# Kernel optimization log

Hardware: AMD Instinct MI355X
Metric: run time of the kernel (lower is better)

The kernel has to match this reference:

```python
import jax, jax.numpy as jnp
import numpy as np

B = 64        # images
P = 100       # boxes per image
C = 256       # q_in_dim
ST = 9        # spatiotemporal_size
M = 2048      # memory entries per image
L = 2         # attention blocks
H = 8         # heads
QK = 256      # qk_out_dim
V = 256       # v_out_dim
FF = 1024     # ff hidden
TEMP = 1.0
SCALER = 1.0 / (TEMP * float(np.sqrt(QK // H)))
EPS = 1e-5


def _ln(x, g, b):
    mu = x.mean(-1, keepdims=True)
    var = ((x - mu) ** 2).mean(-1, keepdims=True)
    return (x - mu) * jax.lax.rsqrt(var + EPS) * g + b


def setup_inputs() -> dict:
    key = jax.random.key(0)
    ks = jax.random.split(key, 32)
    s = 0.02
    KV = C + ST
    d = {
        "features": jax.random.normal(ks[0], (B * P, C, 7, 7), jnp.float32),
        "memory": jax.random.normal(ks[1], (B, M, KV), jnp.float32),
        "Wq": jax.random.normal(ks[2], (L, C, QK), jnp.float32) * s,
        "bq": jnp.zeros((L, QK), jnp.float32),
        "Wk": jax.random.normal(ks[3], (L, KV, QK), jnp.float32) * s,
        "bk": jnp.zeros((L, QK), jnp.float32),
        "Wv": jax.random.normal(ks[4], (L, KV, V), jnp.float32) * s,
        "bv": jnp.zeros((L, V), jnp.float32),
        "Wf": jax.random.normal(ks[5], (L, V, C), jnp.float32) * s,
        "bf": jnp.zeros((L, C), jnp.float32),
        "g1": jnp.ones((L, C), jnp.float32),
        "be1": jnp.zeros((L, C), jnp.float32),
        "g2": jnp.ones((L, C), jnp.float32),
        "be2": jnp.zeros((L, C), jnp.float32),
        "W1": jax.random.normal(ks[6], (L, C, FF), jnp.float32) * s,
        "b1": jnp.zeros((L, FF), jnp.float32),
        "W2": jax.random.normal(ks[7], (L, FF, C), jnp.float32) * s,
        "b2": jnp.zeros((L, C), jnp.float32),
        "Wp1": jax.random.normal(ks[8], (C, FF), jnp.float32) * s,
        "bp1": jnp.zeros((FF,), jnp.float32),
        "Wp2": jax.random.normal(ks[9], (FF, C), jnp.float32) * s,
        "bp2": jnp.zeros((C,), jnp.float32),
        "boxes_per_image": P,
    }
    return d


def reference(features, memory, Wq, bq, Wk, bk, Wv, bv, Wf, bf,
              g1, be1, g2, be2, W1, b1, W2, b2, Wp1, bp1, Wp2, bp2,
              boxes_per_image):
    nb, nm = memory.shape[0], memory.shape[1]
    p = boxes_per_image
    # avg_pool2d(kernel=7) on 7x7 -> spatial mean
    z = features.mean(axis=(2, 3))  # [N, C]
    for i in range(Wq.shape[0]):
        zb = z.reshape(nb, p, -1)                              # [B,P,C]
        q = (zb @ Wq[i] + bq[i]).reshape(nb, p, H, -1)         # [B,P,H,dh]
        k = (memory @ Wk[i] + bk[i]).reshape(nb, nm, H, -1)    # [B,M,H,dh]
        v = (memory @ Wv[i] + bv[i]).reshape(nb, nm, H, -1)
        w = jax.nn.softmax(jnp.einsum('bphd,bmhd->bphm', q, k) * SCALER, axis=-1)
        wv = jnp.einsum('bphm,bmhd->bphd', w, v).reshape(nb, p, -1)
        f = (wv @ Wf[i] + bf[i]).reshape(nb * p, -1)           # [N,C]
        z = _ln(z + f, g1[i], be1[i])
        ff = jnp.maximum(z @ W1[i] + b1[i], 0.0) @ W2[i] + b2[i]
        z = _ln(z + ff, g2[i], be2[i])
    z = jnp.maximum(z @ Wp1 + bp1, 0.0) @ Wp2 + bp2            # ff_post
    return features + z[:, :, None, None]
```

## Files before the change

kernel.cpp:

```cpp
#include <hip/hip_runtime.h>
#include <hip/hip_bf16.h>

typedef __hip_bfloat16 bf16;
typedef float f32x4 __attribute__((ext_vector_type(4)));
typedef short s16x8 __attribute__((ext_vector_type(8)));

#define SCALER_F 0.17677669529663687f

__global__ __launch_bounds__(256) void pool_kernel(
    const float* __restrict__ feat, float* __restrict__ z, bf16* __restrict__ zb) {
  __shared__ float ls[12544];
  const int n = blockIdx.x, t = threadIdx.x;
  const float* fp = feat + (long)n * 12544;
#pragma unroll
  for (int e = t, i = 0; i < 49; i++, e += 256) ls[e] = fp[e];
  __syncthreads();
  float s = 0.f;
  const float* r = ls + t * 49;
#pragma unroll
  for (int i = 0; i < 49; i++) s += r[i];
  s *= (1.f / 49.f);
  z[n * 256 + t] = s;
  zb[n * 256 + t] = __float2bfloat16(s);
}

__global__ __launch_bounds__(64) void transpose_bf(
    const float* __restrict__ src, bf16* __restrict__ dst, int K, int N, int Kpad) {
  const int n = blockIdx.x, t = threadIdx.x;
  for (int k = t; k < Kpad; k += 64)
    dst[(long)n * Kpad + k] = __float2bfloat16(k < K ? src[(long)k * N + n] : 0.f);
}

__global__ __launch_bounds__(64) void conv_mem(
    const float* __restrict__ mem, bf16* __restrict__ mb) {
  const long r = blockIdx.x;
  const int t = threadIdx.x;
  for (int c = t; c < 288; c += 64)
    mb[r * 288 + c] = __float2bfloat16(c < 265 ? mem[r * 265 + c] : 0.f);
}

__global__ void concat_bias(const float* __restrict__ bk, const float* __restrict__ bv,
                            float* __restrict__ kvbias) {
  int i = blockIdx.x * 256 + threadIdx.x;
  if (i < 1024) {
    int l = i >> 9, c = i & 511;
    kvbias[i] = (c < 256) ? bk[l * 256 + c] : bv[l * 256 + c - 256];
  }
}

__global__ __launch_bounds__(256, 2) void gemm_bt(
    const bf16* __restrict__ A, const bf16* __restrict__ Bt,
    const float* __restrict__ bias, float* __restrict__ Cf, bf16* __restrict__ Cb,
    int K, int lda, int ldb, int ldc, float scale, int relu) {
  __shared__ bf16 Als[128 * 32];
  __shared__ bf16 Bls[128 * 32];
  const int m0 = blockIdx.x * 128;
  const int n0 = blockIdx.y * 128;
  const int t = threadIdx.x;
  const int w = t >> 6, lane = t & 63;
  const int rw = (w >> 1) * 64, cw = (w & 1) * 64;
  const int l15 = lane & 15, quad = lane >> 4;

  f32x4 zero4 = {0.f, 0.f, 0.f, 0.f};
  f32x4 acc[4][4];
#pragma unroll
  for (int i = 0; i < 4; i++)
#pragma unroll
    for (int j = 0; j < 4; j++) acc[i][j] = zero4;

  const bf16* Ab = A + (long)m0 * lda;
  const bf16* Bb = Bt + (long)n0 * ldb;
  const int r1 = t >> 2, s1 = t & 3;

  for (int k0 = 0; k0 < K; k0 += 32) {
    __syncthreads();
    __builtin_amdgcn_global_load_lds(
        (const __attribute__((address_space(1))) void*)(Ab + (long)r1 * lda + k0 + s1 * 8),
        (__attribute__((address_space(3))) void*)(Als + t * 8), 16, 0, 0);
    __builtin_amdgcn_global_load_lds(
        (const __attribute__((address_space(1))) void*)(Ab + (long)(r1 + 64) * lda + k0 + s1 * 8),
        (__attribute__((address_space(3))) void*)(Als + 2048 + t * 8), 16, 0, 0);
    __builtin_amdgcn_global_load_lds(
        (const __attribute__((address_space(1))) void*)(Bb + (long)r1 * ldb + k0 + s1 * 8),
        (__attribute__((address_space(3))) void*)(Bls + t * 8), 16, 0, 0);
    __builtin_amdgcn_global_load_lds(
        (const __attribute__((address_space(1))) void*)(Bb + (long)(r1 + 64) * ldb + k0 + s1 * 8),
        (__attribute__((address_space(3))) void*)(Bls + 2048 + t * 8), 16, 0, 0);
    __syncthreads();

    s16x8 af[4], bfr[4];
#pragma unroll
    for (int i = 0; i < 4; i++) {
      af[i]  = *(const s16x8*)(Als + (rw + i * 16 + l15) * 32 + quad * 8);
      bfr[i] = *(const s16x8*)(Bls + (cw + i * 16 + l15) * 32 + quad * 8);
    }
#pragma unroll
    for (int i = 0; i < 4; i++)
#pragma unroll
      for (int j = 0; j < 4; j++)
        acc[i][j] = __builtin_amdgcn_mfma_f32_16x16x32_bf16(af[i], bfr[j], acc[i][j], 0, 0, 0);
  }

#pragma unroll
  for (int i = 0; i < 4; i++) {
    const int row = m0 + rw + i * 16 + quad * 4;
#pragma unroll
    for (int j = 0; j < 4; j++) {
      const int col = n0 + cw + j * 16 + l15;
      const float bvv = bias ? bias[col] : 0.f;
#pragma unroll
      for (int r = 0; r < 4; r++) {
        float v = (acc[i][j][r] + bvv) * scale;
        if (relu) v = fmaxf(v, 0.f);
        const long off = (long)(row + r) * ldc + col;
        if (Cb) Cb[off] = __float2bfloat16(v);
        else    Cf[off] = v;
      }
    }
  }
}

__global__ __launch_bounds__(256) void attn_kernel(
    const bf16* __restrict__ q, const bf16* __restrict__ kv, bf16* __restrict__ wv) {
  const int h = blockIdx.x;
  const int b = blockIdx.y;
  const int t = threadIdx.x;
  const int w = t >> 6, lane = t & 63;
  const int l15 = lane & 15, quad = lane >> 4;

  __shared__ bf16 Kls[64 * 32];
  __shared__ bf16 Vtls[32 * 72];
  __shared__ bf16 Pls[4][16 * 72];

  s16x8 aQ[2];
  f32x4 zero4 = {0.f, 0.f, 0.f, 0.f};
  f32x4 o[2][2];
  float lsum[2][4];
#pragma unroll
  for (int i = 0; i < 2; i++) {
    o[i][0] = zero4; o[i][1] = zero4;
#pragma unroll
    for (int r = 0; r < 4; r++) lsum[i][r] = 0.f;
  }
#pragma unroll
  for (int qt = 0; qt < 2; qt++) {
    const int row = (2 * w + qt) * 16 + l15;
    s16x8 tmp = {0, 0, 0, 0, 0, 0, 0, 0};
    if (row < 100)
      tmp = *(const s16x8*)(q + ((long)(b * 100 + row)) * 256 + h * 32 + quad * 8);
    aQ[qt] = tmp;
  }

  const bf16* kvb = kv + (long)b * 2048 * 512;
  const int sr = t >> 2, ss = t & 3;

  for (int mc = 0; mc < 2048; mc += 64) {
    __syncthreads();
    {
      const uint4 gk = *(const uint4*)(kvb + (long)(mc + sr) * 512 + h * 32 + ss * 8);
      *(uint4*)(Kls + sr * 32 + ss * 8) = gk;
      const uint4 gv = *(const uint4*)(kvb + (long)(mc + sr) * 512 + 256 + h * 32 + ss * 8);
      const bf16* vs = (const bf16*)&gv;
#pragma unroll
      for (int j = 0; j < 8; j++) Vtls[(ss * 8 + j) * 72 + sr] = vs[j];
    }
    __syncthreads();

    s16x8 bk[4], bv00, bv01, bv10, bv11;
#pragma unroll
    for (int f = 0; f < 4; f++)
      bk[f] = *(const s16x8*)(Kls + (f * 16 + l15) * 32 + quad * 8);
    bv00 = *(const s16x8*)(Vtls + l15 * 72 + quad * 8);
    bv01 = *(const s16x8*)(Vtls + l15 * 72 + 32 + quad * 8);
    bv10 = *(const s16x8*)(Vtls + (16 + l15) * 72 + quad * 8);
    bv11 = *(const s16x8*)(Vtls + (16 + l15) * 72 + 32 + quad * 8);

#pragma unroll
    for (int qt = 0; qt < 2; qt++) {
      f32x4 s_[4];
#pragma unroll
      for (int f = 0; f < 4; f++)
        s_[f] = __builtin_amdgcn_mfma_f32_16x16x32_bf16(aQ[qt], bk[f], zero4, 0, 0, 0);
#pragma unroll
      for (int f = 0; f < 4; f++) {
#pragma unroll
        for (int r = 0; r < 4; r++) {
          const float pv = __expf(s_[f][r]);
          lsum[qt][r] += pv;
          Pls[w][(quad * 4 + r) * 72 + f * 16 + l15] = __float2bfloat16(pv);
        }
      }
      __threadfence_block();
      const s16x8 aP0 = *(const s16x8*)(&Pls[w][0] + l15 * 72 + quad * 8);
      const s16x8 aP1 = *(const s16x8*)(&Pls[w][0] + l15 * 72 + 32 + quad * 8);
      o[qt][0] = __builtin_amdgcn_mfma_f32_16x16x32_bf16(aP0, bv00, o[qt][0], 0, 0, 0);
      o[qt][0] = __builtin_amdgcn_mfma_f32_16x16x32_bf16(aP1, bv01, o[qt][0], 0, 0, 0);
      o[qt][1] = __builtin_amdgcn_mfma_f32_16x16x32_bf16(aP0, bv10, o[qt][1], 0, 0, 0);
      o[qt][1] = __builtin_amdgcn_mfma_f32_16x16x32_bf16(aP1, bv11, o[qt][1], 0, 0, 0);
    }
  }

#pragma unroll
  for (int qt = 0; qt < 2; qt++) {
    const int gq = (2 * w + qt) * 16;
#pragma unroll
    for (int r = 0; r < 4; r++) {
      float l = lsum[qt][r];
      l += __shfl_xor(l, 1); l += __shfl_xor(l, 2);
      l += __shfl_xor(l, 4); l += __shfl_xor(l, 8);
      const float inv = 1.f / l;
      const int qrow = gq + quad * 4 + r;
      if (qrow < 100) {
        const long base = ((long)(b * 100 + qrow)) * 256 + h * 32;
        wv[base + l15]      = __float2bfloat16(o[qt][0][r] * inv);
        wv[base + 16 + l15] = __float2bfloat16(o[qt][1][r] * inv);
      }
    }
  }
}

__global__ __launch_bounds__(64) void ln_kernel(
    float* __restrict__ z, const float* __restrict__ d,
    const float* __restrict__ g, const float* __restrict__ be, bf16* __restrict__ zb) {
  const int row = blockIdx.x, t = threadIdx.x;
  float4 x = *(const float4*)(z + (long)row * 256 + t * 4);
  const float4 dd = *(const float4*)(d + (long)row * 256 + t * 4);
  x.x += dd.x; x.y += dd.y; x.z += dd.z; x.w += dd.w;
  float s1 = x.x + x.y + x.z + x.w;
  float s2 = x.x * x.x + x.y * x.y + x.z * x.z + x.w * x.w;
#pragma unroll
  for (int m = 1; m < 64; m <<= 1) {
    s1 += __shfl_xor(s1, m);
    s2 += __shfl_xor(s2, m);
  }
  const float mu = s1 * (1.f / 256.f);
  const float var = s2 * (1.f / 256.f) - mu * mu;
  const float rs = rsqrtf(var + 1e-5f);
  const float4 gg = *(const float4*)(g + t * 4);
  const float4 bb = *(const float4*)(be + t * 4);
  float4 y;
  y.x = (x.x - mu) * rs * gg.x + bb.x;
  y.y = (x.y - mu) * rs * gg.y + bb.y;
  y.z = (x.z - mu) * rs * gg.z + bb.z;
  y.w = (x.w - mu) * rs * gg.w + bb.w;
  *(float4*)(z + (long)row * 256 + t * 4) = y;
  bf16* zo = zb + (long)row * 256 + t * 4;
  zo[0] = __float2bfloat16(y.x); zo[1] = __float2bfloat16(y.y);
  zo[2] = __float2bfloat16(y.z); zo[3] = __float2bfloat16(y.w);
}

__global__ __launch_bounds__(256) void final_add(
    const float* __restrict__ feat, const float* __restrict__ zp, float* __restrict__ out) {
  const int n = blockIdx.x, t = threadIdx.x;
  const long base = (long)n * 12544;
#pragma unroll
  for (int idx = t, i = 0; i < 49; i++, idx += 256) {
    const int c = idx / 49;
    out[base + idx] = feat[base + idx] + zp[n * 256 + c];
  }
}

extern "C" void kernel_launch(void* const* d_in, const int* in_sizes, int n_in,
                              void* d_out, int out_size, void* d_ws, size_t ws_size,
                              hipStream_t stream) {
  (void)in_sizes; (void)n_in; (void)out_size; (void)ws_size;
  const float* features = (const float*)d_in[0];
  const float* memory_  = (const float*)d_in[1];
  const float* Wq_  = (const float*)d_in[2];
  const float* bq_  = (const float*)d_in[3];
  const float* Wk_  = (const float*)d_in[4];
  const float* bk_  = (const float*)d_in[5];
  const float* Wv_  = (const float*)d_in[6];
  const float* bv_  = (const float*)d_in[7];
  const float* Wf_  = (const float*)d_in[8];
  const float* bf_  = (const float*)d_in[9];
  const float* g1_  = (const float*)d_in[10];
  const float* be1_ = (const float*)d_in[11];
  const float* g2_  = (const float*)d_in[12];
  const float* be2_ = (const float*)d_in[13];
  const float* W1_  = (const float*)d_in[14];
  const float* b1_  = (const float*)d_in[15];
  const float* W2_  = (const float*)d_in[16];
  const float* b2_  = (const float*)d_in[17];
  const float* Wp1_ = (const float*)d_in[18];
  const float* bp1_ = (const float*)d_in[19];
  const float* Wp2_ = (const float*)d_in[20];
  const float* bp2_ = (const float*)d_in[21];
  float* out = (float*)d_out;

  char* p = (char*)d_ws;
  auto alloc = [&](size_t bytes) {
    char* r = p;
    p += (bytes + 255) & ~(size_t)255;
    return r;
  };
  float* z     = (float*)alloc((size_t)6400 * 256 * 4);
  float* fb    = (float*)alloc((size_t)6400 * 256 * 4);
  bf16*  zb    = (bf16*)alloc((size_t)6400 * 256 * 2);
  bf16*  qb    = (bf16*)alloc((size_t)6400 * 256 * 2);
  bf16*  wvb   = (bf16*)alloc((size_t)6400 * 256 * 2);
  bf16*  hb    = (bf16*)alloc((size_t)6400 * 1024 * 2);
  bf16*  memb  = (bf16*)alloc((size_t)131072 * 288 * 2);
  bf16*  kvbuf = (bf16*)alloc((size_t)131072 * 512 * 2);
  bf16*  wkvT  = (bf16*)alloc((size_t)2 * 512 * 288 * 2);
  bf16*  wqT   = (bf16*)alloc((size_t)2 * 256 * 256 * 2);
  bf16*  wfT   = (bf16*)alloc((size_t)2 * 256 * 256 * 2);
  bf16*  w1T   = (bf16*)alloc((size_t)2 * 1024 * 256 * 2);
  bf16*  w2T   = (bf16*)alloc((size_t)2 * 256 * 1024 * 2);
  bf16*  wp1T  = (bf16*)alloc((size_t)1024 * 256 * 2);
  bf16*  wp2T  = (bf16*)alloc((size_t)256 * 1024 * 2);
  float* kvbias = (float*)alloc((size_t)1024 * 4);

  conv_mem<<<131072, 64, 0, stream>>>(memory_, memb);
  for (int l = 0; l < 2; l++) {
    transpose_bf<<<256, 64, 0, stream>>>(Wk_ + (long)l * 265 * 256, wkvT + (long)l * 512 * 288, 265, 256, 288);
    transpose_bf<<<256, 64, 0, stream>>>(Wv_ + (long)l * 265 * 256, wkvT + (long)l * 512 * 288 + 256 * 288, 265, 256, 288);
    transpose_bf<<<256, 64, 0, stream>>>(Wq_ + (long)l * 256 * 256, wqT + (long)l * 256 * 256, 256, 256, 256);
    transpose_bf<<<256, 64, 0, stream>>>(Wf_ + (long)l * 256 * 256, wfT + (long)l * 256 * 256, 256, 256, 256);
    transpose_bf<<<1024, 64, 0, stream>>>(W1_ + (long)l * 256 * 1024, w1T + (long)l * 1024 * 256, 256, 1024, 256);
    transpose_bf<<<256, 64, 0, stream>>>(W2_ + (long)l * 1024 * 256, w2T + (long)l * 256 * 1024, 1024, 256, 1024);
  }
  transpose_bf<<<1024, 64, 0, stream>>>(Wp1_, wp1T, 256, 1024, 256);
  transpose_bf<<<256, 64, 0, stream>>>(Wp2_, wp2T, 1024, 256, 1024);
  concat_bias<<<4, 256, 0, stream>>>(bk_, bv_, kvbias);

  pool_kernel<<<6400, 256, 0, stream>>>(features, z, zb);

  for (int l = 0; l < 2; l++) {
    gemm_bt<<<dim3(1024, 4), 256, 0, stream>>>(memb, wkvT + (long)l * 512 * 288,
        kvbias + l * 512, nullptr, kvbuf, 288, 288, 288, 512, 1.f, 0);
    gemm_bt<<<dim3(50, 2), 256, 0, stream>>>(zb, wqT + (long)l * 256 * 256,
        bq_ + l * 256, nullptr, qb, 256, 256, 256, 256, SCALER_F, 0);
    attn_kernel<<<dim3(8, 64), 256, 0, stream>>>(qb, kvbuf, wvb);
    gemm_bt<<<dim3(50, 2), 256, 0, stream>>>(wvb, wfT + (long)l * 256 * 256,
        bf_ + l * 256, fb, nullptr, 256, 256, 256, 256, 1.f, 0);
    ln_kernel<<<6400, 64, 0, stream>>>(z, fb, g1_ + l * 256, be1_ + l * 256, zb);
    gemm_bt<<<dim3(50, 8), 256, 0, stream>>>(zb, w1T + (long)l * 1024 * 256,
        b1_ + l * 1024, nullptr, hb, 256, 256, 256, 1024, 1.f, 1);
    gemm_bt<<<dim3(50, 2), 256, 0, stream>>>(hb, w2T + (long)l * 256 * 1024,
        b2_ + l * 256, fb, nullptr, 1024, 1024, 1024, 256, 1.f, 0);
    ln_kernel<<<6400, 64, 0, stream>>>(z, fb, g2_ + l * 256, be2_ + l * 256, zb);
  }

  gemm_bt<<<dim3(50, 8), 256, 0, stream>>>(zb, wp1T, bp1_, nullptr, hb,
      256, 256, 256, 1024, 1.f, 1);
  gemm_bt<<<dim3(50, 2), 256, 0, stream>>>(hb, wp2T, bp2_, fb,
      nullptr, 1024, 1024, 1024, 256, 1.f, 0);

  final_add<<<6400, 256, 0, stream>>>(features, fb, out);
}
```

Measured before the change: 1.325 ms.

## Fuse prep kernels, batch KV projections, double-buffer attention, vectorize epilogues

Merges the memory conversion, weight transposes and bias concat into one prep kernel with vectorized memory reads. Runs both layers' K/V projections as a single wider GEMM into a 1024-column buffer. Double-buffers K/V tiles in the attention kernel so the next tile's global loads overlap compute. Swaps MFMA operand order so the GEMM epilogue writes 4-wide vectors, and vectorizes the pool and final-add kernels. Costs a larger KV buffer and a strided layer offset in attention.

Result: faster. 1.261 ms (-4.8%).

```diff
diff --git a/kernel.cpp b/kernel.cpp
--- a/kernel.cpp
+++ b/kernel.cpp
@@ -4,16 +4,98 @@
 typedef __hip_bfloat16 bf16;
 typedef float f32x4 __attribute__((ext_vector_type(4)));
 typedef short s16x8 __attribute__((ext_vector_type(8)));
+typedef unsigned short u16x4 __attribute__((ext_vector_type(4)));
 
 #define SCALER_F 0.17677669529663687f
+
+#define MEM_BLKS 33920
+#define PAD_BLKS 11776
+
+__global__ __launch_bounds__(256) void prep_kernel(
+    const float* __restrict__ mem, bf16* __restrict__ mb,
+    const float* __restrict__ Wq, const float* __restrict__ Wk,
+    const float* __restrict__ Wv, const float* __restrict__ Wf,
+    const float* __restrict__ W1, const float* __restrict__ W2,
+    const float* __restrict__ Wp1, const float* __restrict__ Wp2,
+    const float* __restrict__ bk, const float* __restrict__ bv,
+    bf16* __restrict__ wqT, bf16* __restrict__ wkvT, bf16* __restrict__ wfT,
+    bf16* __restrict__ w1T, bf16* __restrict__ w2T,
+    bf16* __restrict__ wp1T, bf16* __restrict__ wp2T,
+    float* __restrict__ kvbias) {
+  int bid = blockIdx.x;
+  const int t = threadIdx.x;
+  if (bid < MEM_BLKS) {
+    const long g4 = (long)bid * 256 + t;
+    const f32x4 v = *(const f32x4*)(mem + g4 * 4);
+    long g = g4 * 4;
+    unsigned r = (unsigned)(g / 265);
+    unsigned c = (unsigned)(g - (long)r * 265);
+#pragma unroll
+    for (int j = 0; j < 4; j++) {
+      mb[(long)r * 288 + c] = __float2bfloat16(v[j]);
+      if (++c == 265) { c = 0; r++; }
+    }
+    return;
+  }
+  bid -= MEM_BLKS;
+  if (bid < PAD_BLKS) {
+    const int p = bid * 256 + t;
+    const int r = p / 23, c = 265 + p % 23;
+    mb[(long)r * 288 + c] = __float2bfloat16(0.f);
+    return;
+  }
+  bid -= PAD_BLKS;
+  const float* src; bf16* dst; int K, N, n, Kpad;
+  if (bid < 1024) {
+    const int l = bid >> 9, pt = (bid >> 8) & 1; n = bid & 255;
+    src = (pt ? Wv : Wk) + (long)l * 265 * 256;
+    dst = wkvT + (long)l * 512 * 288 + (long)pt * 256 * 288;
+    K = 265; N = 256; Kpad = 288;
+  } else if (bid < 1536) {
+    const int i2 = bid - 1024, l = i2 >> 8; n = i2 & 255;
+    src = Wq + (long)l * 65536; dst = wqT + (long)l * 65536;
+    K = 256; N = 256; Kpad = 256;
+  } else if (bid < 2048) {
+    const int i2 = bid - 1536, l = i2 >> 8; n = i2 & 255;
+    src = Wf + (long)l * 65536; dst = wfT + (long)l * 65536;
+    K = 256; N = 256; Kpad = 256;
+  } else if (bid < 4096) {
+    const int i2 = bid - 2048, l = i2 >> 10; n = i2 & 1023;
+    src = W1 + (long)l * 262144; dst = w1T + (long)l * 262144;
+    K = 256; N = 1024; Kpad = 256;
+  } else if (bid < 4608) {
+    const int i2 = bid - 4096, l = i2 >> 8; n = i2 & 255;
+    src = W2 + (long)l * 262144; dst = w2T + (long)l * 262144;
+    K = 1024; N = 256; Kpad = 1024;
+  } else if (bid < 5632) {
+    n = bid - 4608; src = Wp1; dst = wp1T; K = 256; N = 1024; Kpad = 256;
+  } else if (bid < 5888) {
+    n = bid - 5632; src = Wp2; dst = wp2T; K = 1024; N = 256; Kpad = 1024;
+  } else {
+    for (int i = t; i < 1024; i += 256) {
+      const int l = i >> 9, c = i & 511;
+      kvbias[i] = (c < 256) ? bk[l * 256 + c] : bv[l * 256 + c - 256];
+    }
+    return;
+  }
+  for (int k = t; k < Kpad; k += 256)
+    dst[(long)n * Kpad + k] = __float2bfloat16(k < K ? src[(long)k * N + n] : 0.f);
+}
 
 __global__ __launch_bounds__(256) void pool_kernel(
     const float* __restrict__ feat, float* __restrict__ z, bf16* __restrict__ zb) {
   __shared__ float ls[12544];
   const int n = blockIdx.x, t = threadIdx.x;
-  const float* fp = feat + (long)n * 12544;
-#pragma unroll
-  for (int e = t, i = 0; i < 49; i++, e += 256) ls[e] = fp[e];
+  const f32x4* f4 = (const f32x4*)(feat + (long)n * 12544);
+#pragma unroll
+  for (int i = 0; i < 12; i++) {
+    const int e = i * 256 + t;
+    *(f32x4*)&ls[e * 4] = f4[e];
+  }
+  if (t < 64) {
+    const int e = 3072 + t;
+    *(f32x4*)&ls[e * 4] = f4[e];
+  }
   __syncthreads();
   float s = 0.f;
   const float* r = ls + t * 49;
@@ -22,30 +104,6 @@
   s *= (1.f / 49.f);
   z[n * 256 + t] = s;
   zb[n * 256 + t] = __float2bfloat16(s);
-}
-
-__global__ __launch_bounds__(64) void transpose_bf(
-    const float* __restrict__ src, bf16* __restrict__ dst, int K, int N, int Kpad) {
-  const int n = blockIdx.x, t = threadIdx.x;
-  for (int k = t; k < Kpad; k += 64)
-    dst[(long)n * Kpad + k] = __float2bfloat16(k < K ? src[(long)k * N + n] : 0.f);
-}
-
-__global__ __launch_bounds__(64) void conv_mem(
-    const float* __restrict__ mem, bf16* __restrict__ mb) {
-  const long r = blockIdx.x;
-  const int t = threadIdx.x;
-  for (int c = t; c < 288; c += 64)
-    mb[r * 288 + c] = __float2bfloat16(c < 265 ? mem[r * 265 + c] : 0.f);
-}
-
-__global__ void concat_bias(const float* __restrict__ bk, const float* __restrict__ bv,
-                            float* __restrict__ kvbias) {
-  int i = blockIdx.x * 256 + threadIdx.x;
-  if (i < 1024) {
-    int l = i >> 9, c = i & 511;
-    kvbias[i] = (c < 256) ? bk[l * 256 + c] : bv[l * 256 + c - 256];
-  }
 }
 
 __global__ __launch_bounds__(256, 2) void gemm_bt(
@@ -98,38 +156,50 @@
     for (int i = 0; i < 4; i++)
 #pragma unroll
       for (int j = 0; j < 4; j++)
-        acc[i][j] = __builtin_amdgcn_mfma_f32_16x16x32_bf16(af[i], bfr[j], acc[i][j], 0, 0, 0);
+        acc[i][j] = __builtin_amdgcn_mfma_f32_16x16x32_bf16(bfr[j], af[i], acc[i][j], 0, 0, 0);
   }
 
 #pragma unroll
   for (int i = 0; i < 4; i++) {
-    const int row = m0 + rw + i * 16 + quad * 4;
+    const long rb = (long)(m0 + rw + i * 16 + l15) * ldc;
 #pragma unroll
     for (int j = 0; j < 4; j++) {
-      const int col = n0 + cw + j * 16 + l15;
-      const float bvv = bias ? bias[col] : 0.f;
+      const int colb = n0 + cw + j * 16 + quad * 4;
+      f32x4 bv4 = {0.f, 0.f, 0.f, 0.f};
+      if (bias) bv4 = *(const f32x4*)(bias + colb);
+      f32x4 v;
 #pragma unroll
       for (int r = 0; r < 4; r++) {
-        float v = (acc[i][j][r] + bvv) * scale;
-        if (relu) v = fmaxf(v, 0.f);
-        const long off = (long)(row + r) * ldc + col;
-        if (Cb) Cb[off] = __float2bfloat16(v);
-        else    Cf[off] = v;
+        float x = (acc[i][j][r] + bv4[r]) * scale;
+        if (relu) x = fmaxf(x, 0.f);
+        v[r] = x;
       }
+      if (Cb) {
+        u16x4 u;
+#pragma unroll
+        for (int r = 0; r < 4; r++) {
+          bf16 tb = __float2bfloat16(v[r]);
+          u[r] = *(unsigned short*)&tb;
+        }
+        *(u16x4*)(Cb + rb + colb) = u;
+      } else {
+        *(f32x4*)(Cf + rb + colb) = v;
+      }
     }
   }
 }
 
 __global__ __launch_bounds__(256) void attn_kernel(
-    const bf16* __restrict__ q, const bf16* __restrict__ kv, bf16* __restrict__ wv) {
+    const bf16* __restrict__ q, const bf16* __restrict__ kv, bf16* __restrict__ wv,
+    int loff) {
   const int h = blockIdx.x;
   const int b = blockIdx.y;
   const int t = threadIdx.x;
   const int w = t >> 6, lane = t & 63;
   const int l15 = lane & 15, quad = lane >> 4;
 
-  __shared__ bf16 Kls[64 * 32];
-  __shared__ bf16 Vtls[32 * 72];
+  __shared__ bf16 Kls[2][64 * 32];
+  __shared__ bf16 Vtls[2][32 * 72];
   __shared__ bf16 Pls[4][16 * 72];
 
   s16x8 aQ[2];
@@ -151,29 +221,36 @@
     aQ[qt] = tmp;
   }
 
-  const bf16* kvb = kv + (long)b * 2048 * 512;
+  const bf16* kvb = kv + (long)b * 2048 * 1024 + loff;
   const int sr = t >> 2, ss = t & 3;
 
+  {
+    const uint4 gk = *(const uint4*)(kvb + (long)sr * 1024 + h * 32 + ss * 8);
+    *(uint4*)(&Kls[0][sr * 32 + ss * 8]) = gk;
+    const uint4 gv = *(const uint4*)(kvb + (long)sr * 1024 + 256 + h * 32 + ss * 8);
+    const bf16* vs = (const bf16*)&gv;
+#pragma unroll
+    for (int j = 0; j < 8; j++) Vtls[0][(ss * 8 + j) * 72 + sr] = vs[j];
+  }
+  __syncthreads();
+
+  int cur = 0;
   for (int mc = 0; mc < 2048; mc += 64) {
-    __syncthreads();
-    {
-      const uint4 gk = *(const uint4*)(kvb + (long)(mc + sr) * 512 + h * 32 + ss * 8);
-      *(uint4*)(Kls + sr * 32 + ss * 8) = gk;
-      const uint4 gv = *(const uint4*)(kvb + (long)(mc + sr) * 512 + 256 + h * 32 + ss * 8);
-      const bf16* vs = (const bf16*)&gv;
-#pragma unroll
-      for (int j = 0; j < 8; j++) Vtls[(ss * 8 + j) * 72 + sr] = vs[j];
-    }
-    __syncthreads();
+    uint4 gk, gv;
+    const bool more = (mc + 64) < 2048;
+    if (more) {
+      gk = *(const uint4*)(kvb + (long)(mc + 64 + sr) * 1024 + h * 32 + ss * 8);
+      gv = *(const uint4*)(kvb + (long)(mc + 64 + sr) * 1024 + 256 + h * 32 + ss * 8);
+    }
 
     s16x8 bk[4], bv00, bv01, bv10, bv11;
 #pragma unroll
     for (int f = 0; f < 4; f++)
-      bk[f] = *(const s16x8*)(Kls + (f * 16 + l15) * 32 + quad * 8);
-    bv00 = *(const s16x8*)(Vtls + l15 * 72 + quad * 8);
-    bv01 = *(const s16x8*)(Vtls + l15 * 72 + 32 + quad * 8);
-    bv10 = *(const s16x8*)(Vtls + (16 + l15) * 72 + quad * 8);
-    bv11 = *(const s16x8*)(Vtls + (16 + l15) * 72 + 32 + quad * 8);
+      bk[f] = *(const s16x8*)(&Kls[cur][(f * 16 + l15) * 32 + quad * 8]);
+    bv00 = *(const s16x8*)(&Vtls[cur][l15 * 72 + quad * 8]);
+    bv01 = *(const s16x8*)(&Vtls[cur][l15 * 72 + 32 + quad * 8]);
+    bv10 = *(const s16x8*)(&Vtls[cur][(16 + l15) * 72 + quad * 8]);
+    bv11 = *(const s16x8*)(&Vtls[cur][(16 + l15) * 72 + 32 + quad * 8]);
 
 #pragma unroll
     for (int qt = 0; qt < 2; qt++) {
@@ -198,6 +275,15 @@
       o[qt][1] = __builtin_amdgcn_mfma_f32_16x16x32_bf16(aP0, bv10, o[qt][1], 0, 0, 0);
       o[qt][1] = __builtin_amdgcn_mfma_f32_16x16x32_bf16(aP1, bv11, o[qt][1], 0, 0, 0);
     }
+
+    if (more) {
+      *(uint4*)(&Kls[cur ^ 1][sr * 32 + ss * 8]) = gk;
+      const bf16* vs = (const bf16*)&gv;
+#pragma unroll
+      for (int j = 0; j < 8; j++) Vtls[cur ^ 1][(ss * 8 + j) * 72 + sr] = vs[j];
+    }
+    __syncthreads();
+    cur ^= 1;
   }
 
 #pragma unroll
@@ -251,12 +337,28 @@
 
 __global__ __launch_bounds__(256) void final_add(
     const float* __restrict__ feat, const float* __restrict__ zp, float* __restrict__ out) {
+  __shared__ float zs[256];
   const int n = blockIdx.x, t = threadIdx.x;
-  const long base = (long)n * 12544;
-#pragma unroll
-  for (int idx = t, i = 0; i < 49; i++, idx += 256) {
-    const int c = idx / 49;
-    out[base + idx] = feat[base + idx] + zp[n * 256 + c];
+  zs[t] = zp[n * 256 + t];
+  __syncthreads();
+  const f32x4* f4 = (const f32x4*)(feat + (long)n * 12544);
+  f32x4* o4 = (f32x4*)(out + (long)n * 12544);
+#pragma unroll
+  for (int i = 0; i < 12; i++) {
+    const int e = i * 256 + t;
+    f32x4 v = f4[e];
+    const int g = e * 4;
+    v[0] += zs[g / 49]; v[1] += zs[(g + 1) / 49];
+    v[2] += zs[(g + 2) / 49]; v[3] += zs[(g + 3) / 49];
+    o4[e] = v;
+  }
+  if (t < 64) {
+    const int e = 3072 + t;
+    f32x4 v = f4[e];
+    const int g = e * 4;
+    v[0] += zs[g / 49]; v[1] += zs[(g + 1) / 49];
+    v[2] += zs[(g + 2) / 49]; v[3] += zs[(g + 3) / 49];
+    o4[e] = v;
   }
 }
 
@@ -301,7 +403,7 @@
   bf16*  wvb   = (bf16*)alloc((size_t)6400 * 256 * 2);
   bf16*  hb    = (bf16*)alloc((size_t)6400 * 1024 * 2);
   bf16*  memb  = (bf16*)alloc((size_t)131072 * 288 * 2);
-  bf16*  kvbuf = (bf16*)alloc((size_t)131072 * 512 * 2);
+  bf16*  kvbuf = (bf16*)alloc((size_t)131072 * 1024 * 2);
   bf16*  wkvT  = (bf16*)alloc((size_t)2 * 512 * 288 * 2);
   bf16*  wqT   = (bf16*)alloc((size_t)2 * 256 * 256 * 2);
   bf16*  wfT   = (bf16*)alloc((size_t)2 * 256 * 256 * 2);
@@ -311,33 +413,25 @@
   bf16*  wp2T  = (bf16*)alloc((size_t)256 * 1024 * 2);
   float* kvbias = (float*)alloc((size_t)1024 * 4);
 
-  conv_mem<<<131072, 64, 0, stream>>>(memory_, memb);
+  prep_kernel<<<MEM_BLKS + PAD_BLKS + 5889, 256, 0, stream>>>(
+      memory_, memb, Wq_, Wk_, Wv_, Wf_, W1_, W2_, Wp1_, Wp2_, bk_, bv_,
+      wqT, wkvT, wfT, w1T, w2T, wp1T, wp2T, kvbias);
+
+  pool_kernel<<<6400, 256, 0, stream>>>(features, z, zb);
+
+  gemm_bt<<<dim3(1024, 8), 256, 0, stream>>>(memb, wkvT, kvbias,
+      nullptr, kvbuf, 288, 288, 288, 1024, 1.f, 0);
+
   for (int l = 0; l < 2; l++) {
-    transpose_bf<<<256, 64, 0, stream>>>(Wk_ + (long)l * 265 * 256, wkvT + (long)l * 512 * 288, 265, 256, 288);
-    transpose_bf<<<256, 64, 0, stream>>>(Wv_ + (long)l * 265 * 256, wkvT + (long)l * 512 * 288 + 256 * 288, 265, 256, 288);
-    transpose_bf<<<256, 64, 0, stream>>>(Wq_ + (long)l * 256 * 256, wqT + (long)l * 256 * 256, 256, 256, 256);
-    transpose_bf<<<256, 64, 0, stream>>>(Wf_ + (long)l * 256 * 256, wfT + (long)l * 256 * 256, 256, 256, 256);
-    transpose_bf<<<1024, 64, 0, stream>>>(W1_ + (long)l * 256 * 1024, w1T + (long)l * 1024 * 256, 256, 1024, 256);
-    transpose_bf<<<256, 64, 0, stream>>>(W2_ + (long)l * 1024 * 256, w2T + (long)l * 256 * 1024, 1024, 256, 1024);
-  }
-  transpose_bf<<<1024, 64, 0, stream>>>(Wp1_, wp1T, 256, 1024, 256);
-  transpose_bf<<<256, 64, 0, stream>>>(Wp2_, wp2T, 1024, 256, 1024);
-  concat_bias<<<4, 256, 0, stream>>>(bk_, bv_, kvbias);
-
-  pool_kernel<<<6400, 256, 0, stream>>>(features, z, zb);
-
-  for (int l = 0; l < 2; l++) {
-    gemm_bt<<<dim3(1024, 4), 256, 0, stream>>>(memb, wkvT + (long)l * 512 * 288,
-        kvbias + l * 512, nullptr, kvbuf, 288, 288, 288, 512, 1.f, 0);
-    gemm_bt<<<dim3(50, 2), 256, 0, stream>>>(zb, wqT + (long)l * 256 * 256,
+    gemm_bt<<<dim3(50, 2), 256, 0, stream>>>(zb, wqT + (long)l * 65536,
         bq_ + l * 256, nullptr, qb, 256, 256, 256, 256, SCALER_F, 0);
-    attn_kernel<<<dim3(8, 64), 256, 0, stream>>>(qb, kvbuf, wvb);
-    gemm_bt<<<dim3(50, 2), 256, 0, stream>>>(wvb, wfT + (long)l * 256 * 256,
+    attn_kernel<<<dim3(8, 64), 256, 0, stream>>>(qb, kvbuf, wvb, l * 512);
+    gemm_bt<<<dim3(50, 2), 256, 0, stream>>>(wvb, wfT + (long)l * 65536,
         bf_ + l * 256, fb, nullptr, 256, 256, 256, 256, 1.f, 0);
     ln_kernel<<<6400, 64, 0, stream>>>(z, fb, g1_ + l * 256, be1_ + l * 256, zb);
-    gemm_bt<<<dim3(50, 8), 256, 0, stream>>>(zb, w1T + (long)l * 1024 * 256,
+    gemm_bt<<<dim3(50, 8), 256, 0, stream>>>(zb, w1T + (long)l * 262144,
         b1_ + l * 1024, nullptr, hb, 256, 256, 256, 1024, 1.f, 1);
-    gemm_bt<<<dim3(50, 2), 256, 0, stream>>>(hb, w2T + (long)l * 256 * 1024,
+    gemm_bt<<<dim3(50, 2), 256, 0, stream>>>(hb, w2T + (long)l * 262144,
         b2_ + l * 256, fb, nullptr, 1024, 1024, 1024, 256, 1.f, 0);
     ln_kernel<<<6400, 64, 0, stream>>>(z, fb, g2_ + l * 256, be2_ + l * 256, zb);
   }
```
